# Performance work log

Hardware: AMD Instinct MI355X
Metric: run time of the kernel (lower is better)

The kernel has to match this reference:

```python
import jax, jax.numpy as jnp
import numpy as np

SEQ_LEN = 96
D_MODEL = 512
BATCH = 512
FREQ = SEQ_LEN // 2 + 1  # 49
EPS = 1e-5


def setup_inputs() -> dict:
    key = jax.random.key(0)
    ks = jax.random.split(key, 9)
    s = 1.0 / np.sqrt(D_MODEL)
    return {
        "x": jax.random.normal(ks[0], (BATCH, SEQ_LEN, D_MODEL), jnp.float32),
        "freq_weights": jnp.ones((FREQ,), jnp.float32),
        "Wl": jax.random.normal(ks[1], (D_MODEL, D_MODEL), jnp.float32) * s,
        "bl": jax.random.normal(ks[2], (D_MODEL,), jnp.float32) * s,
        "Wh": jax.random.normal(ks[3], (D_MODEL, D_MODEL), jnp.float32) * s,
        "bh": jax.random.normal(ks[4], (D_MODEL,), jnp.float32) * s,
        "Wg": jax.random.normal(ks[5], (2 * D_MODEL, D_MODEL), jnp.float32) * s,
        "bg": jax.random.normal(ks[6], (D_MODEL,), jnp.float32) * s,
        "gamma": jnp.ones((D_MODEL,), jnp.float32),
        "beta": jnp.zeros((D_MODEL,), jnp.float32),
    }


def reference(x, freq_weights, Wl, bl, Wh, bh, Wg, bg, gamma, beta):
    # Batched rfft over seq axis for all channels at once: [B, F, D] complex
    xf = jnp.fft.rfft(x, axis=1)
    xw = xf * freq_weights[None, :, None]
    cutoff = FREQ // 3  # 16 (static)
    idx = jnp.arange(FREQ)[None, :, None]
    x_low_f = jnp.where(idx < cutoff, xw, 0)
    x_high_f = jnp.where(idx >= cutoff, xw, 0)
    x_low = jnp.fft.irfft(x_low_f, n=SEQ_LEN, axis=1)   # [B, S, D]
    x_high = jnp.fft.irfft(x_high_f, n=SEQ_LEN, axis=1)
    x_low = jnp.einsum("bsd,de->bse", x_low, Wl) + bl
    x_high = jnp.einsum("bsd,de->bse", x_high, Wh) + bh
    gate_in = jnp.concatenate([x_low, x_high], axis=-1)  # [B, S, 2D]
    gate = jax.nn.sigmoid(jnp.einsum("bsd,de->bse", gate_in, Wg) + bg)
    out = gate * x_low + (1.0 - gate) * x_high
    y = x + out  # dropout is identity in eval mode
    mu = jnp.mean(y, axis=-1, keepdims=True)
    var = jnp.var(y, axis=-1, keepdims=True)
    return (y - mu) / jnp.sqrt(var + EPS) * gamma + beta
```

## Files before the change

kernel.cpp:

```cpp
#include <hip/hip_runtime.h>

typedef unsigned short u16;
typedef unsigned int u32;

#define SEQ 96
#define DM 512
#define NBATCH 512
#define NFREQ 49
#define CUT 16
#define MROWS (NBATCH * SEQ)
#define MBLK 64

typedef __attribute__((ext_vector_type(8))) short bf16x8;
typedef __attribute__((ext_vector_type(4))) float f32x4;

__device__ __forceinline__ u16 f2bf(float f) {
  u32 u = __float_as_uint(f);
  u32 r = (u + 0x7fffu + ((u >> 16) & 1u)) >> 16;
  return (u16)r;
}
__device__ __forceinline__ float bf2f(u16 u) {
  return __uint_as_float(((u32)u) << 16);
}

__device__ __forceinline__ void g2l16(const void* g, void* l) {
  __builtin_amdgcn_global_load_lds(
      (const __attribute__((address_space(1))) void*)g,
      (__attribute__((address_space(3))) void*)l, 16, 0, 0);
}

__global__ void build_filters_k(const float* __restrict__ w,
                                u16* __restrict__ FlB, u16* __restrict__ FhB) {
  int idx = blockIdx.x * 256 + threadIdx.x;
  if (idx >= SEQ * SEQ) return;
  int s = idx / SEQ, t = idx % SEQ;
  int d = s - t;
  const float scale = 1.0f / (float)SEQ;
  const float w0 = 6.283185307179586f / (float)SEQ;
  float cl = 0.f, ch = 0.f;
  for (int k = 0; k < NFREQ; k++) {
    int m = (k * d) % SEQ;
    if (m < 0) m += SEQ;
    float c = (k == 0 || k == SEQ / 2) ? 1.0f : 2.0f;
    float v = c * w[k] * cosf(w0 * (float)m) * scale;
    if (k < CUT) cl += v; else ch += v;
  }
  FlB[idx] = f2bf(cl);
  FhB[idx] = f2bf(ch);
}

__global__ void __launch_bounds__(256) transpose_w_k(
    const float* __restrict__ W, u16* __restrict__ Wt, int K, int N) {
  __shared__ float t[32][33];
  int k0 = blockIdx.x * 32, n0 = blockIdx.y * 32;
  int tx = threadIdx.x & 31, ty = threadIdx.x >> 5;
  #pragma unroll
  for (int r = 0; r < 32; r += 8)
    t[ty + r][tx] = W[(size_t)(k0 + ty + r) * N + n0 + tx];
  __syncthreads();
  #pragma unroll
  for (int r = 0; r < 32; r += 8)
    Wt[(size_t)(n0 + ty + r) * K + k0 + tx] = f2bf(t[tx][ty + r]);
}

__global__ void __launch_bounds__(256) xt_k(
    const float* __restrict__ x, u16* __restrict__ xT) {
  __shared__ float xs[SEQ * 65];
  int b = blockIdx.x;
  int d0 = blockIdx.y * 64;
  const float* xb = x + (size_t)b * SEQ * DM + d0;
  #pragma unroll
  for (int v = 0; v < 6; v++) {
    int c = v * 256 + threadIdx.x;
    int t = c >> 4, dq = (c & 15) << 2;
    float4 f = *(const float4*)(xb + (size_t)t * DM + dq);
    xs[t * 65 + dq + 0] = f.x;
    xs[t * 65 + dq + 1] = f.y;
    xs[t * 65 + dq + 2] = f.z;
    xs[t * 65 + dq + 3] = f.w;
  }
  __syncthreads();
  u32* outw = (u32*)(xT + ((size_t)b * DM + d0) * SEQ);
  #pragma unroll
  for (int v = 0; v < 12; v++) {
    int c = v * 256 + threadIdx.x;
    int d = c / 48, tw = c % 48;
    int t0 = tw * 2;
    u32 lo = (u32)f2bf(xs[t0 * 65 + d]);
    u32 hi = (u32)f2bf(xs[(t0 + 1) * 65 + d]);
    outw[(size_t)d * 48 + tw] = lo | (hi << 16);
  }
}

__global__ void __launch_bounds__(256) filter_mfma_k(
    const u16* __restrict__ xT, const u16* __restrict__ FlB,
    const u16* __restrict__ FhB, u16* __restrict__ xl, u16* __restrict__ xh) {
  __shared__ __align__(16) u16 lds[128 * SEQ + 2 * SEQ * SEQ];
  u16* Bs = lds;
  u16* As0 = lds + 128 * SEQ;
  int tid = threadIdx.x;
  int lane = tid & 63, w = tid >> 6;
  int b = blockIdx.x, d0 = blockIdx.y * 128;

  const u16* xbase = xT + ((size_t)b * DM + d0) * SEQ;
  #pragma unroll
  for (int it = 0; it < 6; it++) {
    int c = it * 256 + tid;
    int row = c / 12, off = (c % 12) * 8;
    g2l16(xbase + (size_t)row * SEQ + off, (char*)Bs + (((it * 256 + w * 64)) << 4));
  }
  #pragma unroll
  for (int it = 0; it < 9; it++) {
    int c = it * 256 + tid;
    const u16* src = (c < 1152) ? (FlB + c * 8) : (FhB + (c - 1152) * 8);
    g2l16(src, (char*)As0 + ((it * 256 + w * 64) << 4));
  }
  __syncthreads();

  const int l15 = lane & 15, lq = lane >> 4;
  f32x4 acc[2][6][2] = {};
  #pragma unroll
  for (int ks = 0; ks < 3; ks++) {
    int kt = ks * 32;
    bf16x8 bfr[2];
    #pragma unroll
    for (int j = 0; j < 2; j++)
      bfr[j] = *(const bf16x8*)&Bs[(w * 32 + j * 16 + l15) * SEQ + kt + lq * 8];
    #pragma unroll
    for (int f = 0; f < 2; f++)
      #pragma unroll
      for (int i = 0; i < 6; i++) {
        bf16x8 afr = *(const bf16x8*)&As0[f * SEQ * SEQ + (i * 16 + l15) * SEQ + kt + lq * 8];
        #pragma unroll
        for (int j = 0; j < 2; j++)
          acc[f][i][j] = __builtin_amdgcn_mfma_f32_16x16x32_bf16(afr, bfr[j], acc[f][i][j], 0, 0, 0);
      }
  }
  #pragma unroll
  for (int f = 0; f < 2; f++) {
    u16* dst = f ? xh : xl;
    #pragma unroll
    for (int i = 0; i < 6; i++)
      #pragma unroll
      for (int j = 0; j < 2; j++) {
        int d = d0 + w * 32 + j * 16 + l15;
        #pragma unroll
        for (int r = 0; r < 4; r++) {
          int s = i * 16 + lq * 4 + r;
          dst[((size_t)b * SEQ + s) * DM + d] = f2bf(acc[f][i][j][r]);
        }
      }
  }
}

__global__ void __launch_bounds__(256) gemm_proj_mfma_k(
    const u16* __restrict__ xl, const u16* __restrict__ xh,
    const u16* __restrict__ Wlt, const u16* __restrict__ Wht,
    const float* __restrict__ bl, const float* __restrict__ bh,
    u16* __restrict__ yl, u16* __restrict__ yh) {
  const u16* A = blockIdx.z ? xh : xl;
  const u16* Bt = blockIdx.z ? Wht : Wlt;
  const float* bias = blockIdx.z ? bh : bl;
  u16* C = blockIdx.z ? yh : yl;

  __shared__ __align__(16) char stg[2][16384];
  const int m0 = blockIdx.x * 128;
  const int n0 = blockIdx.y * 128;
  const int tid = threadIdx.x;
  const int lane = tid & 63;
  const int w = tid >> 6;
  const int wm = w & 1, wn = w >> 1;
  const int l15 = lane & 15;
  const int lq = lane >> 4;

  f32x4 acc[4][4] = {};

  auto stage = [&](int b, int ks) {
    const int kt = ks * 32;
    #pragma unroll
    for (int it = 0; it < 4; it++) {
      int c = it * 256 + tid;
      int row = (c & 511) >> 2, ce = (c & 3) << 3;
      const u16* src = (c < 512)
          ? A  + (size_t)(m0 + row) * 512 + kt + ce
          : Bt + (size_t)(n0 + row) * 512 + kt + ce;
      g2l16(src, stg[b] + ((it * 256 + w * 64) << 4));
    }
  };

  stage(0, 0);
  __syncthreads();

  #pragma unroll 2
  for (int ks = 0; ks < 16; ks++) {
    const int cur = ks & 1;
    if (ks < 15) stage(cur ^ 1, ks + 1);
    const u16* As = (const u16*)stg[cur];
    const u16* Bs = As + 4096;
    bf16x8 af[4], bf[4];
    #pragma unroll
    for (int i = 0; i < 4; i++)
      af[i] = *(const bf16x8*)&As[(wm * 64 + i * 16 + l15) * 32 + lq * 8];
    #pragma unroll
    for (int j = 0; j < 4; j++)
      bf[j] = *(const bf16x8*)&Bs[(wn * 64 + j * 16 + l15) * 32 + lq * 8];
    #pragma unroll
    for (int i = 0; i < 4; i++)
      #pragma unroll
      for (int j = 0; j < 4; j++)
        acc[i][j] = __builtin_amdgcn_mfma_f32_16x16x32_bf16(af[i], bf[j], acc[i][j], 0, 0, 0);
    __syncthreads();
  }

  #pragma unroll
  for (int j = 0; j < 4; j++) {
    int n = n0 + wn * 64 + j * 16 + l15;
    float bv = bias[n];
    #pragma unroll
    for (int i = 0; i < 4; i++) {
      int mrow = m0 + wm * 64 + i * 16 + lq * 4;
      #pragma unroll
      for (int r = 0; r < 4; r++)
        C[(size_t)(mrow + r) * 512 + n] = f2bf(acc[i][j][r] + bv);
    }
  }
}

__global__ void __launch_bounds__(512, 2) gate_ln_k(
    const u16* __restrict__ yl, const u16* __restrict__ yh,
    const u16* __restrict__ Wgt, const float* __restrict__ bg,
    const float* __restrict__ x, const float* __restrict__ gamma,
    const float* __restrict__ beta, float* __restrict__ out) {
  __shared__ __align__(16) char stg[2][36864];
  __shared__ float redS[MBLK][8];
  __shared__ float redQ[MBLK][8];
  __shared__ float musd[MBLK][2];

  const int tid = threadIdx.x;
  const int lane = tid & 63;
  const int w = tid >> 6;
  const int l15 = lane & 15;
  const int lq = lane >> 4;
  const int m0 = blockIdx.x * MBLK;

  auto stage = [&](int b, int ks) {
    const int kt = ks * 32;
    const int ka = kt & 511;
    const u16* Ak = (ks < 16) ? yl : yh;
    #pragma unroll
    for (int it = 0; it < 5; it++) {
      int c = it * 512 + tid;
      if (it * 512 + w * 64 < 2304) {
        const u16* src;
        if (c < 256) {
          src = Ak + (size_t)(m0 + (c >> 2)) * 512 + ka + ((c & 3) << 3);
        } else {
          int c2 = c - 256;
          src = Wgt + (size_t)(c2 >> 2) * 1024 + kt + ((c2 & 3) << 3);
        }
        g2l16(src, stg[b] + ((it * 512 + w * 64) << 4));
      }
    }
  };

  f32x4 acc[4][4] = {};

  stage(0, 0);
  __syncthreads();

  #pragma unroll 2
  for (int ks = 0; ks < 32; ks++) {
    const int cur = ks & 1;
    if (ks < 31) stage(cur ^ 1, ks + 1);
    const u16* As = (const u16*)stg[cur];
    const u16* Bs = As + 2048;
    bf16x8 af[4], bf[4];
    #pragma unroll
    for (int i = 0; i < 4; i++)
      af[i] = *(const bf16x8*)&As[(i * 16 + l15) * 32 + lq * 8];
    #pragma unroll
    for (int j = 0; j < 4; j++)
      bf[j] = *(const bf16x8*)&Bs[(w * 64 + j * 16 + l15) * 32 + lq * 8];
    #pragma unroll
    for (int i = 0; i < 4; i++)
      #pragma unroll
      for (int j = 0; j < 4; j++)
        acc[i][j] = __builtin_amdgcn_mfma_f32_16x16x32_bf16(af[i], bf[j], acc[i][j], 0, 0, 0);
    __syncthreads();
  }

  #pragma unroll
  for (int j = 0; j < 4; ++j) {
    const int n = w * 64 + j * 16 + l15;
    const float bgv = bg[n];
    #pragma unroll
    for (int i = 0; i < 4; ++i)
      #pragma unroll
      for (int r = 0; r < 4; ++r) {
        const int m = i * 16 + lq * 4 + r;
        const size_t idx = (size_t)(m0 + m) * 512 + n;
        const float z = acc[i][j][r] + bgv;
        const float gv = 1.f / (1.f + __expf(-z));
        const float lv = bf2f(yl[idx]);
        const float hv = bf2f(yh[idx]);
        acc[i][j][r] = x[idx] + gv * lv + (1.f - gv) * hv;
      }
  }

  #pragma unroll
  for (int i = 0; i < 4; ++i)
    #pragma unroll
    for (int r = 0; r < 4; ++r) {
      float s = 0.f, q = 0.f;
      #pragma unroll
      for (int j = 0; j < 4; ++j) {
        const float v = acc[i][j][r];
        s += v; q += v * v;
      }
      #pragma unroll
      for (int off = 8; off; off >>= 1) {
        s += __shfl_xor(s, off);
        q += __shfl_xor(q, off);
      }
      if (l15 == 0) {
        const int m = i * 16 + lq * 4 + r;
        redS[m][w] = s;
        redQ[m][w] = q;
      }
    }
  __syncthreads();

  {
    const int m = tid >> 3, k = tid & 7;
    float s = redS[m][k], q = redQ[m][k];
    #pragma unroll
    for (int off = 4; off; off >>= 1) {
      s += __shfl_xor(s, off);
      q += __shfl_xor(q, off);
    }
    if (k == 0) {
      const float mu = s * (1.f / 512.f);
      const float var = q * (1.f / 512.f) - mu * mu;
      musd[m][0] = mu;
      musd[m][1] = rsqrtf(var + 1e-5f);
    }
  }
  __syncthreads();

  #pragma unroll
  for (int j = 0; j < 4; ++j) {
    const int n = w * 64 + j * 16 + l15;
    const float gm = gamma[n], bt = beta[n];
    #pragma unroll
    for (int i = 0; i < 4; ++i)
      #pragma unroll
      for (int r = 0; r < 4; ++r) {
        const int m = i * 16 + lq * 4 + r;
        const float mu = musd[m][0], inv = musd[m][1];
        out[(size_t)(m0 + m) * 512 + n] = (acc[i][j][r] - mu) * inv * gm + bt;
      }
  }
}

extern "C" void kernel_launch(void* const* d_in, const int* in_sizes, int n_in,
                              void* d_out, int out_size, void* d_ws, size_t ws_size,
                              hipStream_t stream) {
  const float* x     = (const float*)d_in[0];
  const float* fw    = (const float*)d_in[1];
  const float* Wl    = (const float*)d_in[2];
  const float* bl    = (const float*)d_in[3];
  const float* Wh    = (const float*)d_in[4];
  const float* bh    = (const float*)d_in[5];
  const float* Wg    = (const float*)d_in[6];
  const float* bg    = (const float*)d_in[7];
  const float* gamma = (const float*)d_in[8];
  const float* beta  = (const float*)d_in[9];
  float* out = (float*)d_out;

  char* ws = (char*)d_ws;
  u16* FlB = (u16*)ws;
  u16* FhB = FlB + SEQ * SEQ;
  u16* Wlt = (u16*)(ws + 64 * 1024);
  u16* Wht = Wlt + 512 * 512;
  u16* Wgt = Wht + 512 * 512;
  size_t tsz = (size_t)MROWS * 512;
  u16* xl = (u16*)(ws + 4 * 1024 * 1024);
  u16* xh = xl + tsz;
  u16* yl = xh + tsz;
  u16* yh = yl + tsz;
  u16* xT = yl;

  build_filters_k<<<dim3(36), dim3(256), 0, stream>>>(fw, FlB, FhB);
  transpose_w_k<<<dim3(16, 16), dim3(256), 0, stream>>>(Wl, Wlt, 512, 512);
  transpose_w_k<<<dim3(16, 16), dim3(256), 0, stream>>>(Wh, Wht, 512, 512);
  transpose_w_k<<<dim3(32, 16), dim3(256), 0, stream>>>(Wg, Wgt, 1024, 512);
  xt_k<<<dim3(NBATCH, DM / 64), dim3(256), 0, stream>>>(x, xT);
  filter_mfma_k<<<dim3(NBATCH, DM / 128), dim3(256), 0, stream>>>(xT, FlB, FhB, xl, xh);
  gemm_proj_mfma_k<<<dim3(MROWS / 128, 4, 2), dim3(256), 0, stream>>>(
      xl, xh, Wlt, Wht, bl, bh, yl, yh);
  gate_ln_k<<<dim3(MROWS / MBLK), dim3(512), 0, stream>>>(
      yl, yh, Wgt, bg, x, gamma, beta, out);
}
```

Before: 525.4 us.

## Split fused gate+LayerNorm into 128x128-tiled gate GEMM and separate LN kernel

Replaces the fused gate GEMM + LayerNorm kernel, which used 64-row blocks spanning the full 512-wide N dimension, with a 128x128-tiled gate GEMM that writes the pre-norm sum y to an fp32 workspace. A separate row-wise LayerNorm kernel then reads y back and normalizes it. The intent is better operand reuse per block and more blocks in flight for the GEMM. The cost is an extra write and read of a 96MB fp32 intermediate plus one more kernel launch.

```diff
diff --git a/kernel.cpp b/kernel.cpp
--- a/kernel.cpp
+++ b/kernel.cpp
@@ -226,40 +226,32 @@
   }
 }
 
-__global__ void __launch_bounds__(512, 2) gate_ln_k(
+__global__ void __launch_bounds__(256) gate_y_k(
     const u16* __restrict__ yl, const u16* __restrict__ yh,
     const u16* __restrict__ Wgt, const float* __restrict__ bg,
-    const float* __restrict__ x, const float* __restrict__ gamma,
-    const float* __restrict__ beta, float* __restrict__ out) {
-  __shared__ __align__(16) char stg[2][36864];
-  __shared__ float redS[MBLK][8];
-  __shared__ float redQ[MBLK][8];
-  __shared__ float musd[MBLK][2];
-
+    const float* __restrict__ x, float* __restrict__ y) {
+  __shared__ __align__(16) char stg[2][16384];
+  const int m0 = blockIdx.x * 128;
+  const int n0 = blockIdx.y * 128;
   const int tid = threadIdx.x;
   const int lane = tid & 63;
   const int w = tid >> 6;
+  const int wm = w & 1, wn = w >> 1;
   const int l15 = lane & 15;
   const int lq = lane >> 4;
-  const int m0 = blockIdx.x * MBLK;
 
   auto stage = [&](int b, int ks) {
     const int kt = ks * 32;
     const int ka = kt & 511;
     const u16* Ak = (ks < 16) ? yl : yh;
     #pragma unroll
-    for (int it = 0; it < 5; it++) {
-      int c = it * 512 + tid;
-      if (it * 512 + w * 64 < 2304) {
-        const u16* src;
-        if (c < 256) {
-          src = Ak + (size_t)(m0 + (c >> 2)) * 512 + ka + ((c & 3) << 3);
-        } else {
-          int c2 = c - 256;
-          src = Wgt + (size_t)(c2 >> 2) * 1024 + kt + ((c2 & 3) << 3);
-        }
-        g2l16(src, stg[b] + ((it * 512 + w * 64) << 4));
-      }
+    for (int it = 0; it < 4; it++) {
+      int c = it * 256 + tid;
+      int row = (c & 511) >> 2, ce = (c & 3) << 3;
+      const u16* src = (c < 512)
+          ? Ak  + (size_t)(m0 + row) * 512 + ka + ce
+          : Wgt + (size_t)(n0 + row) * 1024 + kt + ce;
+      g2l16(src, stg[b] + ((it * 256 + w * 64) << 4));
     }
   };
 
@@ -273,14 +265,14 @@
     const int cur = ks & 1;
     if (ks < 31) stage(cur ^ 1, ks + 1);
     const u16* As = (const u16*)stg[cur];
-    const u16* Bs = As + 2048;
+    const u16* Bs = As + 4096;
     bf16x8 af[4], bf[4];
     #pragma unroll
     for (int i = 0; i < 4; i++)
-      af[i] = *(const bf16x8*)&As[(i * 16 + l15) * 32 + lq * 8];
+      af[i] = *(const bf16x8*)&As[(wm * 64 + i * 16 + l15) * 32 + lq * 8];
     #pragma unroll
     for (int j = 0; j < 4; j++)
-      bf[j] = *(const bf16x8*)&Bs[(w * 64 + j * 16 + l15) * 32 + lq * 8];
+      bf[j] = *(const bf16x8*)&Bs[(wn * 64 + j * 16 + l15) * 32 + lq * 8];
     #pragma unroll
     for (int i = 0; i < 4; i++)
       #pragma unroll
@@ -290,76 +282,57 @@
   }
 
   #pragma unroll
-  for (int j = 0; j < 4; ++j) {
-    const int n = w * 64 + j * 16 + l15;
+  for (int j = 0; j < 4; j++) {
+    const int n = n0 + wn * 64 + j * 16 + l15;
     const float bgv = bg[n];
     #pragma unroll
-    for (int i = 0; i < 4; ++i)
-      #pragma unroll
-      for (int r = 0; r < 4; ++r) {
-        const int m = i * 16 + lq * 4 + r;
-        const size_t idx = (size_t)(m0 + m) * 512 + n;
+    for (int i = 0; i < 4; i++) {
+      const int mrow = m0 + wm * 64 + i * 16 + lq * 4;
+      #pragma unroll
+      for (int r = 0; r < 4; r++) {
+        const size_t idx = (size_t)(mrow + r) * 512 + n;
         const float z = acc[i][j][r] + bgv;
         const float gv = 1.f / (1.f + __expf(-z));
         const float lv = bf2f(yl[idx]);
         const float hv = bf2f(yh[idx]);
-        acc[i][j][r] = x[idx] + gv * lv + (1.f - gv) * hv;
-      }
-  }
-
-  #pragma unroll
-  for (int i = 0; i < 4; ++i)
-    #pragma unroll
-    for (int r = 0; r < 4; ++r) {
-      float s = 0.f, q = 0.f;
-      #pragma unroll
-      for (int j = 0; j < 4; ++j) {
-        const float v = acc[i][j][r];
-        s += v; q += v * v;
-      }
-      #pragma unroll
-      for (int off = 8; off; off >>= 1) {
-        s += __shfl_xor(s, off);
-        q += __shfl_xor(q, off);
-      }
-      if (l15 == 0) {
-        const int m = i * 16 + lq * 4 + r;
-        redS[m][w] = s;
-        redQ[m][w] = q;
+        y[idx] = x[idx] + gv * lv + (1.f - gv) * hv;
       }
     }
-  __syncthreads();
-
-  {
-    const int m = tid >> 3, k = tid & 7;
-    float s = redS[m][k], q = redQ[m][k];
-    #pragma unroll
-    for (int off = 4; off; off >>= 1) {
-      s += __shfl_xor(s, off);
-      q += __shfl_xor(q, off);
-    }
-    if (k == 0) {
-      const float mu = s * (1.f / 512.f);
-      const float var = q * (1.f / 512.f) - mu * mu;
-      musd[m][0] = mu;
-      musd[m][1] = rsqrtf(var + 1e-5f);
-    }
-  }
-  __syncthreads();
-
-  #pragma unroll
-  for (int j = 0; j < 4; ++j) {
-    const int n = w * 64 + j * 16 + l15;
-    const float gm = gamma[n], bt = beta[n];
-    #pragma unroll
-    for (int i = 0; i < 4; ++i)
-      #pragma unroll
-      for (int r = 0; r < 4; ++r) {
-        const int m = i * 16 + lq * 4 + r;
-        const float mu = musd[m][0], inv = musd[m][1];
-        out[(size_t)(m0 + m) * 512 + n] = (acc[i][j][r] - mu) * inv * gm + bt;
-      }
-  }
+  }
+}
+
+__global__ void __launch_bounds__(256) ln_k(
+    const float* __restrict__ y, const float* __restrict__ gamma,
+    const float* __restrict__ beta, float* __restrict__ out) {
+  __shared__ float red[8];
+  const int r = blockIdx.x;
+  const size_t base = (size_t)r * 512;
+  const int e = threadIdx.x * 2;
+  float2 v = *(const float2*)(y + base + e);
+  float sum = v.x + v.y;
+  float sumsq = v.x * v.x + v.y * v.y;
+  #pragma unroll
+  for (int off = 32; off; off >>= 1) {
+    sum += __shfl_down(sum, off);
+    sumsq += __shfl_down(sumsq, off);
+  }
+  const int wid = threadIdx.x >> 6;
+  if ((threadIdx.x & 63) == 0) {
+    red[wid] = sum;
+    red[4 + wid] = sumsq;
+  }
+  __syncthreads();
+  sum = red[0] + red[1] + red[2] + red[3];
+  sumsq = red[4] + red[5] + red[6] + red[7];
+  const float mu = sum * (1.f / 512.f);
+  const float var = sumsq * (1.f / 512.f) - mu * mu;
+  const float inv = rsqrtf(var + 1e-5f);
+  float2 gm = *(const float2*)(gamma + e);
+  float2 bt = *(const float2*)(beta + e);
+  float2 o;
+  o.x = (v.x - mu) * inv * gm.x + bt.x;
+  o.y = (v.y - mu) * inv * gm.y + bt.y;
+  *(float2*)(out + base + e) = o;
 }
 
 extern "C" void kernel_launch(void* const* d_in, const int* in_sizes, int n_in,
@@ -389,6 +362,7 @@
   u16* yl = xh + tsz;
   u16* yh = yl + tsz;
   u16* xT = yl;
+  float* yf = (float*)xl;
 
   build_filters_k<<<dim3(36), dim3(256), 0, stream>>>(fw, FlB, FhB);
   transpose_w_k<<<dim3(16, 16), dim3(256), 0, stream>>>(Wl, Wlt, 512, 512);
@@ -398,6 +372,7 @@
   filter_mfma_k<<<dim3(NBATCH, DM / 128), dim3(256), 0, stream>>>(xT, FlB, FhB, xl, xh);
   gemm_proj_mfma_k<<<dim3(MROWS / 128, 4, 2), dim3(256), 0, stream>>>(
       xl, xh, Wlt, Wht, bl, bh, yl, yh);
-  gate_ln_k<<<dim3(MROWS / MBLK), dim3(512), 0, stream>>>(
-      yl, yh, Wgt, bg, x, gamma, beta, out);
-}
+  gate_y_k<<<dim3(MROWS / 128, 4), dim3(256), 0, stream>>>(
+      yl, yh, Wgt, bg, x, yf);
+  ln_k<<<dim3(MROWS), dim3(256), 0, stream>>>(yf, gamma, beta, out);
+}
```

After: 561.1 us. 6.8% more time.
